# Performance work log

Measured on AMD Instinct MI355X. Metric: run time of the kernel, lower is better.

The kernel has to match this reference:

```python
import jax, jax.numpy as jnp
import numpy as np

T, B, P, F = 4096, 64, 512, 5
SHARP = 1.0
NEG_LARGE = -1e30


def setup_inputs() -> dict:
    key = jax.random.key(0)
    k1, k2, k3 = jax.random.split(key, 3)
    x = jax.random.normal(k1, (T, B, F), dtype=jnp.float32)
    # seqs index the 4 base features (feature 4 is the 'stay' score)
    seqs = jax.random.randint(k2, (B, P), 0, 4, dtype=jnp.int32)
    # seqlens index into fwd of width P+1, so valid range is [0, P]
    seqlens = jax.random.randint(k3, (B,), 0, P + 1, dtype=jnp.int32)
    return {"x": x, "seqs": seqs, "seqlens": seqlens}


def reference(x, seqs, seqlens):
    nt, nb, nf = x.shape
    ns = seqs.shape[1]
    # initial forward scores: -inf everywhere except position 0
    fwd0 = jnp.full((nb, ns + 1), NEG_LARGE, dtype=x.dtype).at[:, 0].set(0.0)
    xs = x * SHARP  # [T, B, F]

    def step(fwd, xt):
        # stay: emit the 'stay' feature (index 4), keep position
        stay = xt[:, 4][:, None] + fwd  # [B, P+1]
        # move: emit the base at each sequence position, advance by one
        move = jnp.take_along_axis(xt, seqs, axis=1) + fwd[:, :-1]  # [B, P]
        new = stay.at[:, 1:].set(jnp.logaddexp(move, stay[:, 1:]))
        return new, None

    fwd, _ = jax.lax.scan(step, fwd0, xs)
    # score at final position of each sequence, normalized per time step
    return -jnp.take_along_axis(fwd, seqlens[:, None], axis=1) / (nt * SHARP)
```

## Files before the change

kernel.cpp:

```cpp
#include <hip/hip_runtime.h>
#include <hip/hip_fp16.h>


#define TT 4096
#define BB 64
#define PP 512
#define LN2F 0.69314718055994531f
#define LOG2E 1.44269504088896341f

typedef unsigned u32x4 __attribute__((ext_vector_type(4)));

__device__ __forceinline__ unsigned f16_bits(float f) {
    return (unsigned)__half_as_ushort(__float2half(f));
}

__global__ __launch_bounds__(256, 1)
void ctc_prepass(const float* __restrict__ x, u32x4* __restrict__ xq) {
    int j = blockIdx.x * 256 + threadIdx.x;
    int b = j >> 12, t = j & 4095;
    const float* r = x + (size_t)(t * 64 + b) * 5;
    float x0 = r[0], x1 = r[1], x2 = r[2], x3 = r[3], x4 = r[4];
    float w0 = fminf(__expf(x0 - x4), 65000.0f);
    float w1 = fminf(__expf(x1 - x4), 65000.0f);
    float w2 = fminf(__expf(x2 - x4), 65000.0f);
    float w3 = fminf(__expf(x3 - x4), 65000.0f);
    u32x4 o;
    o[0] = f16_bits(w0) | (f16_bits(w1) << 16);
    o[1] = f16_bits(w2) | (f16_bits(w3) << 16);
    o[2] = __float_as_uint(x4);
    o[3] = 0u;
    xq[j] = o;
}

__device__ __forceinline__ void gload_lds16(const void* g, void* l) {
    auto gp = (const __attribute__((address_space(1))) void*)(uintptr_t)g;
    auto lp = (__attribute__((address_space(3))) void*)(uintptr_t)l;
    __builtin_amdgcn_global_load_lds(gp, lp, 16, 0, 0);
}

__device__ __forceinline__ int shl1w_i(int s) {
    return __builtin_amdgcn_update_dpp(s, s, 0x138, 0xF, 0xF, false);
}
__device__ __forceinline__ float shl1w_f(float s) {
    return __int_as_float(shl1w_i(__float_as_int(s)));
}
__device__ __forceinline__ int sh1up_i(int s) {
    return __builtin_amdgcn_update_dpp(s, s, 0x130, 0xF, 0xF, false);
}
__device__ __forceinline__ float sh1up_f(float s) {
    return __int_as_float(sh1up_i(__float_as_int(s)));
}

#define FMA_MIX_LO(acc, s, p)                                              \
    asm("v_fma_mix_f32 %0, %1, %2, %0 op_sel:[0,0,0] op_sel_hi:[0,1,0]"    \
        : "+v"(acc) : "v"(s), "v"(p))
#define FMA_MIX_HI(acc, s, p)                                              \
    asm("v_fma_mix_f32 %0, %1, %2, %0 op_sel:[0,1,0] op_sel_hi:[0,1,0]"    \
        : "+v"(acc) : "v"(s), "v"(p))

__global__ __launch_bounds__(128, 1)
void ctc_scan(const u32x4* __restrict__ xq, const int* __restrict__ seqs,
              const int* __restrict__ seqlens, float* __restrict__ out) {
    __shared__ __align__(16) u32x4 ringF[512];
    __shared__ __align__(16) u32x4 ringB[512];
    __shared__ float garrF[PP + 1];
    __shared__ float garrB[PP + 1];
    __shared__ float lgSh[2];

    const int tid = threadIdx.x;
    const int w = tid >> 6;
    const int l = tid & 63;
    const int b = blockIdx.x;
    const bool lane0 = (l == 0);
    const bool lane63 = (l == 63);

    unsigned ctrl[4];
#pragma unroll
    for (int k = 0; k < 4; ++k) {
        unsigned i0 = (unsigned)seqs[b * PP + 8 * l + 2 * k];
        unsigned i1 = (unsigned)seqs[b * PP + 8 * l + 2 * k + 1];
        ctrl[k] = (2 * i0) | ((2 * i0 + 1) << 8) | ((2 * i1) << 16) | ((2 * i1 + 1) << 24);
    }

    const u32x4* gsrc = xq + (size_t)b * 4096;

    float F[8];
    int M = 0;
    float logs = 0.0f;

    if (w == 0) {
#pragma unroll
        for (int i = 0; i < 8; ++i) F[i] = 0.0f;
#pragma unroll
        for (int c0 = 0; c0 < 4; ++c0)
            gload_lds16(gsrc + c0 * 64 + l, &ringF[c0 * 64 + l]);
        asm volatile("s_waitcnt vmcnt(3)" ::: "memory");

        u32x4 wA[8], wB[8];
#pragma unroll
        for (int i = 0; i < 8; ++i) wA[i] = ringF[i];
        int nrow = 8;

        auto fwin = [&](u32x4 (&cur)[8], u32x4 (&nxt)[8]) {
            const int rb = nrow & 511;
            nrow += 8;
#pragma unroll
            for (int i = 0; i < 8; ++i) nxt[i] = ringF[rb + i];
            asm volatile("" ::: "memory");

            float m = F[0];
#pragma unroll
            for (int i = 1; i < 8; ++i) m = fmaxf(m, F[i]);
            int e2 = ((__float_as_int(m) >> 23) & 0xFF) - 127;
            e2 = (m > 0.0f) ? e2 : 0;
            const int Mp = M + e2;
            const int Mlp = shl1w_i(Mp);
            int dl = (lane0 ? 0 : Mlp) - Mp;
            int dlc = dl > 0 ? dl : 0;
            const int Mnew = Mp + dlc;
            const int sh = Mnew - M;
#pragma unroll
            for (int i = 0; i < 8; ++i) F[i] = ldexpf(F[i], -sh);
            M = Mnew;
            int dn = Mlp - M; dn = dn > 0 ? 0 : dn;
            const float sAx  = lane0 ? 0.0f : ldexpf(1.0f, dn);
            const float cfin = lane0 ? ldexpf(1.0f, -M) : 0.0f;

#pragma unroll
            for (int u = 0; u < 8; ++u) {
                const u32x4 row = cur[u];
                logs += __uint_as_float(row[2]);
                unsigned p0 = __builtin_amdgcn_perm(row[1], row[0], ctrl[0]);
                unsigned p1 = __builtin_amdgcn_perm(row[1], row[0], ctrl[1]);
                unsigned p2 = __builtin_amdgcn_perm(row[1], row[0], ctrl[2]);
                unsigned p3 = __builtin_amdgcn_perm(row[1], row[0], ctrl[3]);
                const float Flr = shl1w_f(F[7]);
                const float fin = fmaf(Flr, sAx, cfin);
                FMA_MIX_HI(F[7], F[6], p3);
                FMA_MIX_LO(F[6], F[5], p3);
                FMA_MIX_HI(F[5], F[4], p2);
                FMA_MIX_LO(F[4], F[3], p2);
                FMA_MIX_HI(F[3], F[2], p1);
                FMA_MIX_LO(F[2], F[1], p1);
                FMA_MIX_HI(F[1], F[0], p0);
                FMA_MIX_LO(F[0], fin,  p0);
            }
        };

#pragma unroll 1
        for (int c = 0; c < 32; ++c) {
            int cs = (c + 4 > 31) ? 31 : (c + 4);
            gload_lds16(gsrc + cs * 64 + l, &ringF[((c + 4) & 7) * 64 + l]);
            asm volatile("s_waitcnt vmcnt(3)" ::: "memory");
#pragma unroll 1
            for (int pr = 0; pr < 4; ++pr) { fwin(wA, wB); fwin(wB, wA); }
        }

#pragma unroll
        for (int i = 0; i < 8; ++i) {
            float v = fmaxf(F[i] * 16777216.0f, 1e-38f);
            garrF[8 * l + 1 + i] = __log2f(v) - 24.0f + (float)M;
        }
        if (lane0) { garrF[0] = 0.0f; lgSh[0] = logs * LOG2E; }
    } else {
        const int sl = seqlens[b];
        const bool b512 = (sl == PP);
#pragma unroll
        for (int k = 0; k < 8; ++k) F[k] = (8 * l + k == sl) ? 1.0f : 0.0f;
#pragma unroll
        for (int c0 = 0; c0 < 4; ++c0) {
            const int cp = 63 - c0;
            gload_lds16(gsrc + cp * 64 + l, &ringB[(cp & 7) * 64 + l]);
        }
        asm volatile("s_waitcnt vmcnt(3)" ::: "memory");

        u32x4 wA[8], wB[8];
#pragma unroll
        for (int i = 0; i < 8; ++i) wA[i] = ringB[511 - i];
        int nbase = 4095 - 8;

        auto bwin = [&](u32x4 (&cur)[8], u32x4 (&nxt)[8]) {
            const int rb = nbase & 511;
            nbase -= 8;
#pragma unroll
            for (int i = 0; i < 8; ++i) nxt[i] = ringB[(rb - i) & 511];
            asm volatile("" ::: "memory");

            float m = F[0];
#pragma unroll
            for (int i = 1; i < 8; ++i) m = fmaxf(m, F[i]);
            int e2 = ((__float_as_int(m) >> 23) & 0xFF) - 127;
            e2 = (m > 0.0f) ? e2 : 0;
            const int Mp = M + e2;
            const int Mup = sh1up_i(Mp);
            int nb = lane63 ? (b512 ? 0 : -1048576) : Mup;
            int dl = nb - Mp;
            int dlc = dl > 0 ? dl : 0;
            const int Mnew = Mp + dlc;
            const int sh = Mnew - M;
#pragma unroll
            for (int i = 0; i < 8; ++i) F[i] = ldexpf(F[i], -sh);
            M = Mnew;
            int dn = Mup - M; dn = dn > 0 ? 0 : dn;
            const float sAx  = lane63 ? 0.0f : ldexpf(1.0f, dn);
            const float cfin = (lane63 && b512) ? ldexpf(1.0f, -M) : 0.0f;

#pragma unroll
            for (int u = 0; u < 8; ++u) {
                const u32x4 row = cur[u];
                logs += __uint_as_float(row[2]);
                unsigned p0 = __builtin_amdgcn_perm(row[1], row[0], ctrl[0]);
                unsigned p1 = __builtin_amdgcn_perm(row[1], row[0], ctrl[1]);
                unsigned p2 = __builtin_amdgcn_perm(row[1], row[0], ctrl[2]);
                unsigned p3 = __builtin_amdgcn_perm(row[1], row[0], ctrl[3]);
                const float Bur = sh1up_f(F[0]);
                const float fin = fmaf(Bur, sAx, cfin);
                FMA_MIX_LO(F[0], F[1], p0);
                FMA_MIX_HI(F[1], F[2], p0);
                FMA_MIX_LO(F[2], F[3], p1);
                FMA_MIX_HI(F[3], F[4], p1);
                FMA_MIX_LO(F[4], F[5], p2);
                FMA_MIX_HI(F[5], F[6], p2);
                FMA_MIX_LO(F[6], F[7], p3);
                FMA_MIX_HI(F[7], fin,  p3);
            }
        };

#pragma unroll 1
        for (int c = 0; c < 32; ++c) {
            int cp = 59 - c; cp = cp < 32 ? 32 : cp;
            gload_lds16(gsrc + cp * 64 + l, &ringB[(cp & 7) * 64 + l]);
            asm volatile("s_waitcnt vmcnt(3)" ::: "memory");
#pragma unroll 1
            for (int pr = 0; pr < 4; ++pr) { bwin(wA, wB); bwin(wB, wA); }
        }

#pragma unroll
        for (int k = 0; k < 8; ++k) {
            float v = fmaxf(F[k] * 16777216.0f, 1e-38f);
            garrB[8 * l + k] = __log2f(v) - 24.0f + (float)M;
        }
        if (lane0) { garrB[PP] = b512 ? 0.0f : -1e30f; lgSh[1] = logs * LOG2E; }
    }

    __syncthreads();

    if (w == 0) {
        float smax = -3.0e38f;
#pragma unroll
        for (int k = 0; k < 9; ++k) {
            const int p = l + (k << 6);
            if (p <= PP) smax = fmaxf(smax, garrF[p] + garrB[p]);
        }
#pragma unroll
        for (int off = 32; off >= 1; off >>= 1)
            smax = fmaxf(smax, __shfl_xor(smax, off));
        float ssum = 0.0f;
#pragma unroll
        for (int k = 0; k < 9; ++k) {
            const int p = l + (k << 6);
            if (p <= PP) ssum += exp2f((garrF[p] + garrB[p]) - smax);
        }
#pragma unroll
        for (int off = 32; off >= 1; off >>= 1)
            ssum += __shfl_xor(ssum, off);
        if (lane0)
            out[b] = -((smax + __log2f(ssum)) + lgSh[0] + lgSh[1]) * LN2F / (float)TT;
    }
}

extern "C" void kernel_launch(void* const* d_in, const int* in_sizes, int n_in,
                              void* d_out, int out_size, void* d_ws, size_t ws_size,
                              hipStream_t stream) {
    const float* x       = (const float*)d_in[0];
    const int*   seqs    = (const int*)d_in[1];
    const int*   seqlens = (const int*)d_in[2];
    float*       out     = (float*)d_out;
    u32x4*       xq      = (u32x4*)d_ws;

    ctc_prepass<<<(TT * BB) / 256, 256, 0, stream>>>(x, xq);
    ctc_scan<<<BB, 128, 0, stream>>>(xq, seqs, seqlens, out);
}
```

Baseline: 164.3 us.

## Split forward and backward scans into separate blocks with a global-memory join kernel

Each batch's forward and backward recursion previously ran as two wavefronts in one 128-thread block. Now they run as separate 64-thread blocks (128 blocks in total), and a third kernel combines the results through a workspace buffer. The aim is to place the two sequential wavefronts on different CUs so each gets a whole CU and its own LDS ring instead of sharing one. The cost is an extra kernel launch and a global-memory round trip for the join.

Measured after the change: 166.8 us. No clear change (+1.5%).

```diff
diff --git a/kernel.cpp b/kernel.cpp
--- a/kernel.cpp
+++ b/kernel.cpp
@@ -7,6 +7,7 @@
 #define PP 512
 #define LN2F 0.69314718055994531f
 #define LOG2E 1.44269504088896341f
+#define JSTRIDE 1040
 
 typedef unsigned u32x4 __attribute__((ext_vector_type(4)));
 
@@ -58,21 +59,17 @@
     asm("v_fma_mix_f32 %0, %1, %2, %0 op_sel:[0,1,0] op_sel_hi:[0,1,0]"    \
         : "+v"(acc) : "v"(s), "v"(p))
 
-__global__ __launch_bounds__(128, 1)
+__global__ __launch_bounds__(64, 1)
 void ctc_scan(const u32x4* __restrict__ xq, const int* __restrict__ seqs,
-              const int* __restrict__ seqlens, float* __restrict__ out) {
-    __shared__ __align__(16) u32x4 ringF[512];
-    __shared__ __align__(16) u32x4 ringB[512];
-    __shared__ float garrF[PP + 1];
-    __shared__ float garrB[PP + 1];
-    __shared__ float lgSh[2];
-
-    const int tid = threadIdx.x;
-    const int w = tid >> 6;
-    const int l = tid & 63;
-    const int b = blockIdx.x;
+              const int* __restrict__ seqlens, float* __restrict__ jbuf) {
+    __shared__ __align__(16) u32x4 ring[512];
+
+    const int b = blockIdx.x >> 1;
+    const int w = blockIdx.x & 1;
+    const int l = threadIdx.x;
     const bool lane0 = (l == 0);
     const bool lane63 = (l == 63);
+    float* const jb = jbuf + (size_t)b * JSTRIDE;
 
     unsigned ctrl[4];
 #pragma unroll
@@ -93,19 +90,19 @@
         for (int i = 0; i < 8; ++i) F[i] = 0.0f;
 #pragma unroll
         for (int c0 = 0; c0 < 4; ++c0)
-            gload_lds16(gsrc + c0 * 64 + l, &ringF[c0 * 64 + l]);
+            gload_lds16(gsrc + c0 * 64 + l, &ring[c0 * 64 + l]);
         asm volatile("s_waitcnt vmcnt(3)" ::: "memory");
 
         u32x4 wA[8], wB[8];
 #pragma unroll
-        for (int i = 0; i < 8; ++i) wA[i] = ringF[i];
+        for (int i = 0; i < 8; ++i) wA[i] = ring[i];
         int nrow = 8;
 
         auto fwin = [&](u32x4 (&cur)[8], u32x4 (&nxt)[8]) {
             const int rb = nrow & 511;
             nrow += 8;
 #pragma unroll
-            for (int i = 0; i < 8; ++i) nxt[i] = ringF[rb + i];
+            for (int i = 0; i < 8; ++i) nxt[i] = ring[rb + i];
             asm volatile("" ::: "memory");
 
             float m = F[0];
@@ -150,7 +147,7 @@
 #pragma unroll 1
         for (int c = 0; c < 32; ++c) {
             int cs = (c + 4 > 31) ? 31 : (c + 4);
-            gload_lds16(gsrc + cs * 64 + l, &ringF[((c + 4) & 7) * 64 + l]);
+            gload_lds16(gsrc + cs * 64 + l, &ring[((c + 4) & 7) * 64 + l]);
             asm volatile("s_waitcnt vmcnt(3)" ::: "memory");
 #pragma unroll 1
             for (int pr = 0; pr < 4; ++pr) { fwin(wA, wB); fwin(wB, wA); }
@@ -159,9 +156,9 @@
 #pragma unroll
         for (int i = 0; i < 8; ++i) {
             float v = fmaxf(F[i] * 16777216.0f, 1e-38f);
-            garrF[8 * l + 1 + i] = __log2f(v) - 24.0f + (float)M;
-        }
-        if (lane0) { garrF[0] = 0.0f; lgSh[0] = logs * LOG2E; }
+            jb[8 * l + 1 + i] = __log2f(v) - 24.0f + (float)M;
+        }
+        if (lane0) { jb[0] = 0.0f; jb[1036] = logs * LOG2E; }
     } else {
         const int sl = seqlens[b];
         const bool b512 = (sl == PP);
@@ -170,20 +167,20 @@
 #pragma unroll
         for (int c0 = 0; c0 < 4; ++c0) {
             const int cp = 63 - c0;
-            gload_lds16(gsrc + cp * 64 + l, &ringB[(cp & 7) * 64 + l]);
+            gload_lds16(gsrc + cp * 64 + l, &ring[(cp & 7) * 64 + l]);
         }
         asm volatile("s_waitcnt vmcnt(3)" ::: "memory");
 
         u32x4 wA[8], wB[8];
 #pragma unroll
-        for (int i = 0; i < 8; ++i) wA[i] = ringB[511 - i];
+        for (int i = 0; i < 8; ++i) wA[i] = ring[511 - i];
         int nbase = 4095 - 8;
 
         auto bwin = [&](u32x4 (&cur)[8], u32x4 (&nxt)[8]) {
             const int rb = nbase & 511;
             nbase -= 8;
 #pragma unroll
-            for (int i = 0; i < 8; ++i) nxt[i] = ringB[(rb - i) & 511];
+            for (int i = 0; i < 8; ++i) nxt[i] = ring[(rb - i) & 511];
             asm volatile("" ::: "memory");
 
             float m = F[0];
@@ -229,7 +226,7 @@
 #pragma unroll 1
         for (int c = 0; c < 32; ++c) {
             int cp = 59 - c; cp = cp < 32 ? 32 : cp;
-            gload_lds16(gsrc + cp * 64 + l, &ringB[(cp & 7) * 64 + l]);
+            gload_lds16(gsrc + cp * 64 + l, &ring[(cp & 7) * 64 + l]);
             asm volatile("s_waitcnt vmcnt(3)" ::: "memory");
 #pragma unroll 1
             for (int pr = 0; pr < 4; ++pr) { bwin(wA, wB); bwin(wB, wA); }
@@ -238,35 +235,38 @@
 #pragma unroll
         for (int k = 0; k < 8; ++k) {
             float v = fmaxf(F[k] * 16777216.0f, 1e-38f);
-            garrB[8 * l + k] = __log2f(v) - 24.0f + (float)M;
-        }
-        if (lane0) { garrB[PP] = b512 ? 0.0f : -1e30f; lgSh[1] = logs * LOG2E; }
-    }
-
-    __syncthreads();
-
-    if (w == 0) {
-        float smax = -3.0e38f;
-#pragma unroll
-        for (int k = 0; k < 9; ++k) {
-            const int p = l + (k << 6);
-            if (p <= PP) smax = fmaxf(smax, garrF[p] + garrB[p]);
-        }
-#pragma unroll
-        for (int off = 32; off >= 1; off >>= 1)
-            smax = fmaxf(smax, __shfl_xor(smax, off));
-        float ssum = 0.0f;
-#pragma unroll
-        for (int k = 0; k < 9; ++k) {
-            const int p = l + (k << 6);
-            if (p <= PP) ssum += exp2f((garrF[p] + garrB[p]) - smax);
-        }
-#pragma unroll
-        for (int off = 32; off >= 1; off >>= 1)
-            ssum += __shfl_xor(ssum, off);
-        if (lane0)
-            out[b] = -((smax + __log2f(ssum)) + lgSh[0] + lgSh[1]) * LN2F / (float)TT;
-    }
+            jb[520 + 8 * l + k] = __log2f(v) - 24.0f + (float)M;
+        }
+        if (lane0) { jb[520 + PP] = b512 ? 0.0f : -1e30f; jb[1037] = logs * LOG2E; }
+    }
+}
+
+__global__ __launch_bounds__(64, 1)
+void ctc_join(const float* __restrict__ jbuf, float* __restrict__ out) {
+    const int b = blockIdx.x;
+    const int l = threadIdx.x;
+    const float* jb = jbuf + (size_t)b * JSTRIDE;
+
+    float smax = -3.0e38f;
+#pragma unroll
+    for (int k = 0; k < 9; ++k) {
+        const int p = l + (k << 6);
+        if (p <= PP) smax = fmaxf(smax, jb[p] + jb[520 + p]);
+    }
+#pragma unroll
+    for (int off = 32; off >= 1; off >>= 1)
+        smax = fmaxf(smax, __shfl_xor(smax, off));
+    float ssum = 0.0f;
+#pragma unroll
+    for (int k = 0; k < 9; ++k) {
+        const int p = l + (k << 6);
+        if (p <= PP) ssum += exp2f((jb[p] + jb[520 + p]) - smax);
+    }
+#pragma unroll
+    for (int off = 32; off >= 1; off >>= 1)
+        ssum += __shfl_xor(ssum, off);
+    if (l == 0)
+        out[b] = -((smax + __log2f(ssum)) + jb[1036] + jb[1037]) * LN2F / (float)TT;
 }
 
 extern "C" void kernel_launch(void* const* d_in, const int* in_sizes, int n_in,
@@ -277,7 +277,9 @@
     const int*   seqlens = (const int*)d_in[2];
     float*       out     = (float*)d_out;
     u32x4*       xq      = (u32x4*)d_ws;
+    float*       jbuf    = (float*)((char*)d_ws + (4u << 20));
 
     ctc_prepass<<<(TT * BB) / 256, 256, 0, stream>>>(x, xq);
-    ctc_scan<<<BB, 128, 0, stream>>>(xq, seqs, seqlens, out);
-}
+    ctc_scan<<<BB * 2, 64, 0, stream>>>(xq, seqs, seqlens, jbuf);
+    ctc_join<<<BB, 64, 0, stream>>>(jbuf, out);
+}
```
